# Kernel optimization log

Hardware: AMD Instinct MI355X
Metric: run time of the kernel (lower is better)

The kernel has to match this reference:

```python
import jax, jax.numpy as jnp
import numpy as np

# ---- static config matching init_kwargs / input_specs ----
B, H, W_IN, IN_CAPS, ATOMS = 2, 48, 48, 8, 16
KER, STRIDE, OUT_CAPS, ROUTINGS = 3, 1, 16, 3


def setup_inputs() -> dict:
    key = jax.random.key(0)
    k1, k2 = jax.random.split(key)
    x = jax.random.normal(k1, (B, H, W_IN, IN_CAPS * (ATOMS + 1)), dtype=jnp.float32)
    # W: [input_num_capsule, num_capsule, 4, 4], he_normal-ish scale (fan_in=16)
    W = jax.random.normal(k2, (IN_CAPS, OUT_CAPS, 4, 4), dtype=jnp.float32) * np.float32((2.0 / 16.0) ** 0.5)
    return {"input_tensor": x, "W": W}


def _kernel_tile(x, k=KER, stride=STRIDE):
    # Equivalent to the depthwise-conv patch-extraction trick + transpose:
    # output [B, Ho, Wo, k*k, C]
    b, h, w, c = x.shape
    ho = (h - k) // stride + 1
    wo = (w - k) // stride + 1
    patches = jnp.stack(
        [x[:, i:i + stride * ho:stride, j:j + stride * wo:stride, :]
         for i in range(k) for j in range(k)],
        axis=3,
    )
    return patches


def _squash(s, eps=1e-7):
    sq = jnp.sum(s * s, axis=-1, keepdims=True)
    return (sq / (1.0 + sq)) * s / jnp.sqrt(sq + eps)


def reference(input_tensor, W):
    t = _kernel_tile(input_tensor)                      # [B,Ho,Wo,kk,C]
    b, ho, wo, kk, c = t.shape
    n = b * ho * wo
    t = t.reshape(n, kk * IN_CAPS, ATOMS + 1)           # [N, kk*in_caps, 17]
    pose = t[..., :ATOMS].reshape(n, kk, IN_CAPS, 4, 4)
    act = t[..., ATOMS].reshape(n, kk * IN_CAPS)        # input capsule activations
    # vote transform: pose @ W per (input capsule -> output capsule)
    votes = jnp.einsum('nkiab,iobc->nkioac', pose, W)
    votes = votes.reshape(n, kk * IN_CAPS, OUT_CAPS, ATOMS)  # [N, kkin, out, 16]
    # iterative routing-by-agreement, weighted by input activation
    logits = jnp.zeros((n, kk * IN_CAPS, OUT_CAPS), dtype=votes.dtype)
    v = None
    for r in range(ROUTINGS):
        coup = jax.nn.softmax(logits, axis=2) * act[:, :, None]
        s = jnp.einsum('nko,nkoe->noe', coup, votes)    # weighted vote sum
        v = _squash(s)                                  # [N, out, 16]
        if r < ROUTINGS - 1:
            logits = logits + jnp.einsum('nkoe,noe->nko', votes, v)
    return v.reshape(b, ho, wo, OUT_CAPS, ATOMS)
```

## Files before the change

kernel.cpp:

```cpp
#include <hip/hip_runtime.h>


#define NPIX 4232
#define NBLK 1058

typedef float v2f __attribute__((ext_vector_type(2)));
typedef float v4f __attribute__((ext_vector_type(4)));

__device__ __forceinline__ v2f lo2(v4f v) { return __builtin_shufflevector(v, v, 0, 1); }
__device__ __forceinline__ v2f hi2(v4f v) { return __builtin_shufflevector(v, v, 2, 3); }
__device__ __forceinline__ v2f fma2(v2f a, v2f b, v2f c) {
    return __builtin_elementwise_fma(a, b, c);
}

template<int CTRL>
__device__ __forceinline__ float dpp_f(float x) {
    return __int_as_float(
        __builtin_amdgcn_update_dpp(0, __float_as_int(x), CTRL, 0xF, 0xF, true));
}
template<int OFF>
__device__ __forceinline__ float swz(float x) {
    return __int_as_float(__builtin_amdgcn_ds_swizzle(__float_as_int(x), OFF));
}

__device__ __forceinline__ int g_row(int o, int ic) {
    return (o * 8 + ic) * 20 + o * 4;
}

__global__ __launch_bounds__(256, 2)
void capsule_routing_kernel(const float* __restrict__ x,
                            const float* __restrict__ Wg,
                            float* __restrict__ out)
{
    __shared__ alignas(16) float pose_t[4][1288];
    __shared__ alignas(16) float coup_s[4][1216];
    __shared__ alignas(16) float g_s[4][2616];

    const int tid  = threadIdx.x;
    const int wid  = tid >> 6;
    const int lane = tid & 63;
    const int o    = lane >> 2;
    const int cq   = lane & 3;

    float* PT = pose_t[wid];
    float* CP = coup_s[wid];
    float* G  = g_s[wid];

    const int bx  = blockIdx.x;
    const int xcd = bx & 7;
    const int sub = bx >> 3;
    const int wgs = (xcd < 2 ? xcd * 133 : 266 + (xcd - 2) * 132) + sub;
    const int n   = wgs * 4 + wid;

    const int b   = n / (46 * 46);
    const int rem = n - b * (46 * 46);
    const int ho  = rem / 46;
    const int wo  = rem - ho * 46;

    v2f w01[8], w23[8];
    #pragma unroll
    for (int i = 0; i < 8; ++i) {
        const v4f wv = *reinterpret_cast<const v4f*>(
            &Wg[((i * 16 + o) * 4 + cq) * 4]);
        w01[i] = lo2(wv);
        w23[i] = hi2(wv);
    }

    #pragma unroll
    for (int p = 0; p < 9; ++p) {
        const int py = p / 3, px = p - py * 3;
        const float* xr = &x[(((b * 48) + ho + py) * 48 + (wo + px)) * 136];
        #pragma unroll
        for (int t = 0; t < 3; ++t) {
            const int cc = lane + t * 64;
            if (t < 2 || cc < 136) {
                const float val = xr[cc];
                const int ic = (cc * 241) >> 12;
                const int aa = cc - ic * 17;
                const int k  = p * 8 + ic;
                if (aa == 16) PT[1216 + k] = val;
                else          PT[aa * 76 + k] = val;
            }
        }
    }
    asm volatile("s_waitcnt lgkmcnt(0)" ::: "memory");

    float lreg[16];
    #pragma unroll
    for (int j = 0; j < 16; ++j) lreg[j] = 0.f;
    float lt0 = 0.f, lt1 = 0.f;

    const int kT  = 64 + (lane >> 3);
    const int icT = lane >> 3;
    const int oT0 = (lane & 7) * 2;

    v2f va01[4], va23[4];

    #pragma unroll 1
    for (int r = 0; r < 3; ++r) {
        const float* cb  = (r == 0) ? (PT + 1216) : (CP + o * 76);
        const float  msc = (r == 0) ? 0.0625f : 1.0f;
        v2f mac[4][4];
        #pragma unroll
        for (int m = 0; m < 4; ++m)
            #pragma unroll
            for (int a = 0; a < 4; ++a) mac[m][a] = v2f{0.f, 0.f};
        #pragma unroll
        for (int p = 0; p < 9; ++p) {
            const v4f c0 = *reinterpret_cast<const v4f*>(cb + 8 * p);
            const v4f c1 = *reinterpret_cast<const v4f*>(cb + 8 * p + 4);
            #pragma unroll
            for (int a = 0; a < 4; ++a) {
                const v4f q0 = *reinterpret_cast<const v4f*>(
                    &PT[(a * 4 + cq) * 76 + 8 * p]);
                const v4f q1 = *reinterpret_cast<const v4f*>(
                    &PT[(a * 4 + cq) * 76 + 8 * p + 4]);
                mac[0][a] = fma2(lo2(c0), lo2(q0), mac[0][a]);
                mac[1][a] = fma2(hi2(c0), hi2(q0), mac[1][a]);
                mac[2][a] = fma2(lo2(c1), lo2(q1), mac[2][a]);
                mac[3][a] = fma2(hi2(c1), hi2(q1), mac[3][a]);
            }
        }
        v2f U01[4], U23[4];
        #pragma unroll
        for (int a = 0; a < 4; ++a) { U01[a] = v2f{0.f,0.f}; U23[a] = v2f{0.f,0.f}; }
        #pragma unroll
        for (int m = 0; m < 4; ++m) {
            #pragma unroll
            for (int a = 0; a < 4; ++a) {
                const v2f m0 = { mac[m][a].x, mac[m][a].x };
                const v2f m1 = { mac[m][a].y, mac[m][a].y };
                U01[a] = fma2(w01[2*m],   m0, U01[a]);
                U23[a] = fma2(w23[2*m],   m0, U23[a]);
                U01[a] = fma2(w01[2*m+1], m1, U01[a]);
                U23[a] = fma2(w23[2*m+1], m1, U23[a]);
            }
        }
        float Z[16];
        #pragma unroll
        for (int a = 0; a < 4; ++a) {
            Z[a*4+0] = U01[a].x * msc;  Z[a*4+1] = U01[a].y * msc;
            Z[a*4+2] = U23[a].x * msc;  Z[a*4+3] = U23[a].y * msc;
        }
        #pragma unroll
        for (int j = 0; j < 16; ++j) {
            Z[j] += dpp_f<0xB1>(Z[j]);
            Z[j] += dpp_f<0x4E>(Z[j]);
        }
        float sq = 0.f;
        #pragma unroll
        for (int j = 0; j < 16; ++j) sq = fmaf(Z[j], Z[j], sq);
        const float ss = sq / ((1.f + sq) * sqrtf(sq + 1e-7f));
        #pragma unroll
        for (int a = 0; a < 4; ++a) {
            va01[a] = v2f{ Z[a*4+0] * ss, Z[a*4+1] * ss };
            va23[a] = v2f{ Z[a*4+2] * ss, Z[a*4+3] * ss };
        }

        if (r < 2) {
            #pragma unroll
            for (int ic = 0; ic < 8; ++ic) {
                #pragma unroll
                for (int a = 0; a < 4; ++a) {
                    const v2f h = fma2(w23[ic], va23[a], w01[ic] * va01[a]);
                    G[g_row(o, ic) + a * 4 + cq] = h.x + h.y;
                }
            }
            float pc[16], pcT[16];
            #pragma unroll
            for (int j = 0; j < 16; ++j) pc[j]  = PT[j * 76 + lane];
            #pragma unroll
            for (int j = 0; j < 16; ++j) pcT[j] = PT[j * 76 + kT];
            const float actk = PT[1216 + lane];
            const float actT = PT[1216 + kT];
            asm volatile("s_waitcnt lgkmcnt(0)" ::: "memory");

            const int icM = lane & 7;
            const v2f q0 = {pc[0],  pc[1]},  q1 = {pc[2],  pc[3]};
            const v2f q2 = {pc[4],  pc[5]},  q3 = {pc[6],  pc[7]};
            const v2f q4 = {pc[8],  pc[9]},  q5 = {pc[10], pc[11]};
            const v2f q6 = {pc[12], pc[13]}, q7 = {pc[14], pc[15]};
            float lg[16];
            #pragma unroll
            for (int oo = 0; oo < 16; ++oo) {
                const v4f* gp = reinterpret_cast<const v4f*>(&G[g_row(oo, icM)]);
                const v4f g0 = gp[0], g1 = gp[1], g2 = gp[2], g3 = gp[3];
                const v2f A  = fma2(q2, lo2(g1), fma2(q4, lo2(g2),
                               fma2(q6, lo2(g3), q0 * lo2(g0))));
                const v2f Bv = fma2(q3, hi2(g1), fma2(q5, hi2(g2),
                               fma2(q7, hi2(g3), q1 * hi2(g0))));
                lreg[oo] += (A.x + A.y) + (Bv.x + Bv.y);
                lg[oo] = lreg[oo];
            }
            float mx = lg[0];
            #pragma unroll
            for (int j = 1; j < 16; ++j) mx = fmaxf(mx, lg[j]);
            float sum = 0.f;
            #pragma unroll
            for (int j = 0; j < 16; ++j) { lg[j] = __expf(lg[j] - mx); sum += lg[j]; }
            const float cs = actk / sum;
            #pragma unroll
            for (int oo = 0; oo < 16; ++oo) CP[oo * 76 + lane] = lg[oo] * cs;

            {
                const v2f t0 = {pcT[0],  pcT[1]},  t1 = {pcT[2],  pcT[3]};
                const v2f t2 = {pcT[4],  pcT[5]},  t3 = {pcT[6],  pcT[7]};
                const v2f t4 = {pcT[8],  pcT[9]},  t5 = {pcT[10], pcT[11]};
                const v2f t6 = {pcT[12], pcT[13]}, t7 = {pcT[14], pcT[15]};
                {
                    const v4f* gp = reinterpret_cast<const v4f*>(&G[g_row(oT0, icT)]);
                    const v4f g0 = gp[0], g1 = gp[1], g2 = gp[2], g3 = gp[3];
                    const v2f A  = fma2(t2, lo2(g1), fma2(t4, lo2(g2),
                                   fma2(t6, lo2(g3), t0 * lo2(g0))));
                    const v2f Bv = fma2(t3, hi2(g1), fma2(t5, hi2(g2),
                                   fma2(t7, hi2(g3), t1 * hi2(g0))));
                    lt0 += (A.x + A.y) + (Bv.x + Bv.y);
                }
                {
                    const v4f* gp = reinterpret_cast<const v4f*>(&G[g_row(oT0 + 1, icT)]);
                    const v4f g0 = gp[0], g1 = gp[1], g2 = gp[2], g3 = gp[3];
                    const v2f A  = fma2(t2, lo2(g1), fma2(t4, lo2(g2),
                                   fma2(t6, lo2(g3), t0 * lo2(g0))));
                    const v2f Bv = fma2(t3, hi2(g1), fma2(t5, hi2(g2),
                                   fma2(t7, hi2(g3), t1 * hi2(g0))));
                    lt1 += (A.x + A.y) + (Bv.x + Bv.y);
                }
                float m2 = fmaxf(lt0, lt1);
                m2 = fmaxf(m2, swz<0x041F>(m2));
                m2 = fmaxf(m2, swz<0x081F>(m2));
                m2 = fmaxf(m2, swz<0x101F>(m2));
                const float e0 = __expf(lt0 - m2);
                const float e1 = __expf(lt1 - m2);
                float s2 = e0 + e1;
                s2 += swz<0x041F>(s2);
                s2 += swz<0x081F>(s2);
                s2 += swz<0x101F>(s2);
                const float csT = actT / s2;
                CP[oT0 * 76 + kT]       = e0 * csT;
                CP[(oT0 + 1) * 76 + kT] = e1 * csT;
            }
            asm volatile("s_waitcnt lgkmcnt(0)" ::: "memory");
        }
    }

    #pragma unroll
    for (int a = 0; a < 4; ++a) {
        const float vo = (cq & 2) ? ((cq & 1) ? va23[a].y : va23[a].x)
                                  : ((cq & 1) ? va01[a].y : va01[a].x);
        out[n * 256 + o * 16 + a * 4 + cq] = vo;
    }
}

extern "C" void kernel_launch(void* const* d_in, const int* in_sizes, int n_in,
                              void* d_out, int out_size, void* d_ws, size_t ws_size,
                              hipStream_t stream) {
    const float* x  = (const float*)d_in[0];
    const float* Wt = (const float*)d_in[1];
    float* outp = (float*)d_out;
    capsule_routing_kernel<<<dim3(NBLK), dim3(256), 0, stream>>>(x, Wt, outp);
}
```

Before: 95.18 us.

## Alias coupling and agreement LDS buffers, halve block size, vectorize G stores

The separate coupling buffer is merged into the per-wave G buffer, and each block now runs two waves instead of four, so per-block LDS drops sharply and more waves can be resident per CU. The G tile is stored transposed, so each lane writes one float4 instead of four scalars, and the dot-product macro reads it in the matching order. The pose-column loads (pc, pcT, activations) are hoisted out of the routing loop so they are read from LDS only once. The costs are more live registers across the loop, and correctness now relies on in-order LDS access within a wave because the same buffer is reused for both G and the couplings.

```diff
diff --git a/kernel.cpp b/kernel.cpp
--- a/kernel.cpp
+++ b/kernel.cpp
@@ -2,7 +2,7 @@
 
 
 #define NPIX 4232
-#define NBLK 1058
+#define NBLK 2116
 
 typedef float v2f __attribute__((ext_vector_type(2)));
 typedef float v4f __attribute__((ext_vector_type(4)));
@@ -27,14 +27,13 @@
     return (o * 8 + ic) * 20 + o * 4;
 }
 
-__global__ __launch_bounds__(256, 2)
+__global__ __launch_bounds__(128, 2)
 void capsule_routing_kernel(const float* __restrict__ x,
                             const float* __restrict__ Wg,
                             float* __restrict__ out)
 {
-    __shared__ alignas(16) float pose_t[4][1288];
-    __shared__ alignas(16) float coup_s[4][1216];
-    __shared__ alignas(16) float g_s[4][2616];
+    __shared__ alignas(16) float pose_t[2][1288];
+    __shared__ alignas(16) float g_buf[2][2616];
 
     const int tid  = threadIdx.x;
     const int wid  = tid >> 6;
@@ -43,14 +42,13 @@
     const int cq   = lane & 3;
 
     float* PT = pose_t[wid];
-    float* CP = coup_s[wid];
-    float* G  = g_s[wid];
+    float* GB = g_buf[wid];
 
     const int bx  = blockIdx.x;
     const int xcd = bx & 7;
     const int sub = bx >> 3;
-    const int wgs = (xcd < 2 ? xcd * 133 : 266 + (xcd - 2) * 132) + sub;
-    const int n   = wgs * 4 + wid;
+    const int wgs = (xcd < 4 ? xcd * 265 : 1060 + (xcd - 4) * 264) + sub;
+    const int n   = wgs * 2 + wid;
 
     const int b   = n / (46 * 46);
     const int rem = n - b * (46 * 46);
@@ -85,20 +83,44 @@
     }
     asm volatile("s_waitcnt lgkmcnt(0)" ::: "memory");
 
-    float lreg[16];
-    #pragma unroll
-    for (int j = 0; j < 16; ++j) lreg[j] = 0.f;
-    float lt0 = 0.f, lt1 = 0.f;
-
     const int kT  = 64 + (lane >> 3);
     const int icT = lane >> 3;
     const int oT0 = (lane & 7) * 2;
+    const int icM = lane & 7;
+
+    float pc[16], pcT[16];
+    #pragma unroll
+    for (int j = 0; j < 16; ++j) pc[j]  = PT[j * 76 + lane];
+    #pragma unroll
+    for (int j = 0; j < 16; ++j) pcT[j] = PT[j * 76 + kT];
+    const float actk = PT[1216 + lane];
+    const float actT = PT[1216 + kT];
+    asm volatile("s_waitcnt lgkmcnt(0)" ::: "memory");
+
+    float lreg[16];
+    #pragma unroll
+    for (int j = 0; j < 16; ++j) lreg[j] = 0.f;
+    float lt0 = 0.f, lt1 = 0.f;
 
     v2f va01[4], va23[4];
+
+    #define GDOT(P, gp, accum) do {                                          \
+        const v4f b0 = (gp)[0], b1 = (gp)[1], b2 = (gp)[2], b3 = (gp)[3];    \
+        v2f acc2 = {0.f, 0.f};                                               \
+        acc2 = fma2(v2f{(P)[0], (P)[4]},  lo2(b0), acc2);                    \
+        acc2 = fma2(v2f{(P)[8], (P)[12]}, hi2(b0), acc2);                    \
+        acc2 = fma2(v2f{(P)[1], (P)[5]},  lo2(b1), acc2);                    \
+        acc2 = fma2(v2f{(P)[9], (P)[13]}, hi2(b1), acc2);                    \
+        acc2 = fma2(v2f{(P)[2], (P)[6]},  lo2(b2), acc2);                    \
+        acc2 = fma2(v2f{(P)[10],(P)[14]}, hi2(b2), acc2);                    \
+        acc2 = fma2(v2f{(P)[3], (P)[7]},  lo2(b3), acc2);                    \
+        acc2 = fma2(v2f{(P)[11],(P)[15]}, hi2(b3), acc2);                    \
+        accum += acc2.x + acc2.y;                                            \
+    } while (0)
 
     #pragma unroll 1
     for (int r = 0; r < 3; ++r) {
-        const float* cb  = (r == 0) ? (PT + 1216) : (CP + o * 76);
+        const float* cb  = (r == 0) ? (PT + 1216) : (GB + o * 76);
         const float  msc = (r == 0) ? 0.0625f : 1.0f;
         v2f mac[4][4];
         #pragma unroll
@@ -160,38 +182,30 @@
         if (r < 2) {
             #pragma unroll
             for (int ic = 0; ic < 8; ++ic) {
+                v4f gv;
                 #pragma unroll
                 for (int a = 0; a < 4; ++a) {
                     const v2f h = fma2(w23[ic], va23[a], w01[ic] * va01[a]);
-                    G[g_row(o, ic) + a * 4 + cq] = h.x + h.y;
+                    gv[a] = h.x + h.y;
                 }
-            }
-            float pc[16], pcT[16];
-            #pragma unroll
-            for (int j = 0; j < 16; ++j) pc[j]  = PT[j * 76 + lane];
-            #pragma unroll
-            for (int j = 0; j < 16; ++j) pcT[j] = PT[j * 76 + kT];
-            const float actk = PT[1216 + lane];
-            const float actT = PT[1216 + kT];
+                *reinterpret_cast<v4f*>(&GB[g_row(o, ic) + cq * 4]) = gv;
+            }
             asm volatile("s_waitcnt lgkmcnt(0)" ::: "memory");
 
-            const int icM = lane & 7;
-            const v2f q0 = {pc[0],  pc[1]},  q1 = {pc[2],  pc[3]};
-            const v2f q2 = {pc[4],  pc[5]},  q3 = {pc[6],  pc[7]};
-            const v2f q4 = {pc[8],  pc[9]},  q5 = {pc[10], pc[11]};
-            const v2f q6 = {pc[12], pc[13]}, q7 = {pc[14], pc[15]};
             float lg[16];
             #pragma unroll
             for (int oo = 0; oo < 16; ++oo) {
-                const v4f* gp = reinterpret_cast<const v4f*>(&G[g_row(oo, icM)]);
-                const v4f g0 = gp[0], g1 = gp[1], g2 = gp[2], g3 = gp[3];
-                const v2f A  = fma2(q2, lo2(g1), fma2(q4, lo2(g2),
-                               fma2(q6, lo2(g3), q0 * lo2(g0))));
-                const v2f Bv = fma2(q3, hi2(g1), fma2(q5, hi2(g2),
-                               fma2(q7, hi2(g3), q1 * hi2(g0))));
-                lreg[oo] += (A.x + A.y) + (Bv.x + Bv.y);
+                const v4f* gp = reinterpret_cast<const v4f*>(&GB[g_row(oo, icM)]);
+                GDOT(pc, gp, lreg[oo]);
                 lg[oo] = lreg[oo];
             }
+            {
+                const v4f* gp0 = reinterpret_cast<const v4f*>(&GB[g_row(oT0, icT)]);
+                GDOT(pcT, gp0, lt0);
+                const v4f* gp1 = reinterpret_cast<const v4f*>(&GB[g_row(oT0 + 1, icT)]);
+                GDOT(pcT, gp1, lt1);
+            }
+
             float mx = lg[0];
             #pragma unroll
             for (int j = 1; j < 16; ++j) mx = fmaxf(mx, lg[j]);
@@ -200,31 +214,9 @@
             for (int j = 0; j < 16; ++j) { lg[j] = __expf(lg[j] - mx); sum += lg[j]; }
             const float cs = actk / sum;
             #pragma unroll
-            for (int oo = 0; oo < 16; ++oo) CP[oo * 76 + lane] = lg[oo] * cs;
+            for (int oo = 0; oo < 16; ++oo) GB[oo * 76 + lane] = lg[oo] * cs;
 
             {
-                const v2f t0 = {pcT[0],  pcT[1]},  t1 = {pcT[2],  pcT[3]};
-                const v2f t2 = {pcT[4],  pcT[5]},  t3 = {pcT[6],  pcT[7]};
-                const v2f t4 = {pcT[8],  pcT[9]},  t5 = {pcT[10], pcT[11]};
-                const v2f t6 = {pcT[12], pcT[13]}, t7 = {pcT[14], pcT[15]};
-                {
-                    const v4f* gp = reinterpret_cast<const v4f*>(&G[g_row(oT0, icT)]);
-                    const v4f g0 = gp[0], g1 = gp[1], g2 = gp[2], g3 = gp[3];
-                    const v2f A  = fma2(t2, lo2(g1), fma2(t4, lo2(g2),
-                                   fma2(t6, lo2(g3), t0 * lo2(g0))));
-                    const v2f Bv = fma2(t3, hi2(g1), fma2(t5, hi2(g2),
-                                   fma2(t7, hi2(g3), t1 * hi2(g0))));
-                    lt0 += (A.x + A.y) + (Bv.x + Bv.y);
-                }
-                {
-                    const v4f* gp = reinterpret_cast<const v4f*>(&G[g_row(oT0 + 1, icT)]);
-                    const v4f g0 = gp[0], g1 = gp[1], g2 = gp[2], g3 = gp[3];
-                    const v2f A  = fma2(t2, lo2(g1), fma2(t4, lo2(g2),
-                                   fma2(t6, lo2(g3), t0 * lo2(g0))));
-                    const v2f Bv = fma2(t3, hi2(g1), fma2(t5, hi2(g2),
-                                   fma2(t7, hi2(g3), t1 * hi2(g0))));
-                    lt1 += (A.x + A.y) + (Bv.x + Bv.y);
-                }
                 float m2 = fmaxf(lt0, lt1);
                 m2 = fmaxf(m2, swz<0x041F>(m2));
                 m2 = fmaxf(m2, swz<0x081F>(m2));
@@ -236,8 +228,9 @@
                 s2 += swz<0x081F>(s2);
                 s2 += swz<0x101F>(s2);
                 const float csT = actT / s2;
-                CP[oT0 * 76 + kT]       = e0 * csT;
-                CP[(oT0 + 1) * 76 + kT] = e1 * csT;
+                GB[oT0 * 76 + kT]       = e0 * csT;
+                GB[(oT0 + 1) * 76 + kT] = e1 * csT;
+                lt0 = lt0; lt1 = lt1;
             }
             asm volatile("s_waitcnt lgkmcnt(0)" ::: "memory");
         }
@@ -257,5 +250,5 @@
     const float* x  = (const float*)d_in[0];
     const float* Wt = (const float*)d_in[1];
     float* outp = (float*)d_out;
-    capsule_routing_kernel<<<dim3(NBLK), dim3(256), 0, stream>>>(x, Wt, outp);
-}
+    capsule_routing_kernel<<<dim3(NBLK), dim3(128), 0, stream>>>(x, Wt, outp);
+}
```

Result: faster. 89.86 us (-5.6%).
